# Kernel tuning notes

Hardware: AMD Instinct MI355X
Metric: run time of the kernel (lower is better)

## Reference

```python
import jax, jax.numpy as jnp
import numpy as np

D_IN, D_HID, D_OUT = 256, 256, 10  # mlp dims (init_kwargs)


def mlp(params, x):
    # x: [D_IN] (single sample, matching fnet_single's unsqueeze/squeeze)
    h = jnp.tanh(x @ params["W1"] + params["b1"])
    h = jnp.tanh(h @ params["W2"] + params["b2"])
    return h @ params["W3"] + params["b3"]  # [D_OUT]


def setup_inputs() -> dict:
    key = jax.random.key(0)
    ks = jax.random.split(key, 8)
    rn = lambda k, shp, scale: (jax.random.normal(k, shp, jnp.float32) * scale)
    return {
        "x1": jax.random.normal(ks[0], (64, D_IN), jnp.float32),
        "x2": jax.random.normal(ks[1], (64, D_IN), jnp.float32),
        "W1": rn(ks[2], (D_IN, D_HID), 1.0 / np.sqrt(D_IN)),
        "b1": jnp.zeros((D_HID,), jnp.float32),
        "W2": rn(ks[3], (D_HID, D_HID), 1.0 / np.sqrt(D_HID)),
        "b2": jnp.zeros((D_HID,), jnp.float32),
        "W3": rn(ks[4], (D_HID, D_OUT), 1.0 / np.sqrt(D_HID)),
        "b3": jnp.zeros((D_OUT,), jnp.float32),
    }


def reference(x1, x2, W1, b1, W2, b2, W3, b3):
    params = {"W1": W1, "b1": b1, "W2": W2, "b2": b2, "W3": W3, "b3": b3}
    # vmap(jacrev(fnet_single), (None, 0)): per-sample Jacobian w.r.t. every param tensor
    jac_fn = jax.vmap(jax.jacrev(mlp, argnums=0), in_axes=(None, 0))
    jac1 = jax.tree_util.tree_leaves(jac_fn(params, x1))  # list of [N, O, *pshape]
    jac2 = jax.tree_util.tree_leaves(jac_fn(params, x2))  # list of [M, O, *pshape]
    # flatten(2): [N, O, f] per param tensor
    j1 = [j.reshape(j.shape[0], j.shape[1], -1) for j in jac1]
    j2 = [j.reshape(j.shape[0], j.shape[1], -1) for j in jac2]
    # per-param einsum, then sum over param tensors (== stack(...).sum(0))
    result = sum(jnp.einsum("Naf,Mbf->NMab", a, b) for a, b in zip(j1, j2))
    return result  # [N, M, O, O]
```

## Files before the change

### kernel.cpp

```cpp
#include <hip/hip_runtime.h>

#define NS 64
#define D  256
#define O  10

typedef unsigned short u16;
typedef __attribute__((ext_vector_type(8))) short bf16x8;
typedef __attribute__((ext_vector_type(4))) float f32x4;

__device__ __forceinline__ u16 f2bf(float f) {
    union { float f; unsigned u; } v; v.f = f;
    unsigned r = v.u + 0x7FFFu + ((v.u >> 16) & 1u);
    return (u16)(r >> 16);
}
__device__ __forceinline__ float bf2f(u16 h) {
    union { unsigned u; float f; } v; v.u = ((unsigned)h) << 16;
    return v.f;
}

__global__ __launch_bounds__(512) void prep1_kernel(
    const float* __restrict__ x1, const float* __restrict__ x2,
    const float* __restrict__ W1, const float* __restrict__ b1,
    const float* __restrict__ W2, const float* __restrict__ b2,
    const float* __restrict__ W3,
    float* __restrict__ h1o, float* __restrict__ S1o,
    float* __restrict__ h2o, u16* __restrict__ G2b,
    float* __restrict__ W2T)
{
    int t = threadIdx.x;
    if (blockIdx.x >= 128) {
        int blk = blockIdx.x - 128;
        int bxT = blk & 7, byT = blk >> 3;
        __shared__ float tile[32][33];
        int txT = t & 31, tyT = t >> 5;
        #pragma unroll
        for (int r = 0; r < 2; ++r)
            tile[tyT + 16 * r][txT] = W2[(byT * 32 + tyT + 16 * r) * D + bxT * 32 + txT];
        __syncthreads();
        #pragma unroll
        for (int r = 0; r < 2; ++r)
            W2T[(bxT * 32 + tyT + 16 * r) * D + byT * 32 + txT] = tile[txT][tyT + 16 * r];
        return;
    }

    int s = blockIdx.x;
    const float* x = (s < NS) ? (x1 + s * D) : (x2 + (s - NS) * D);
    int tt = t & 255, half = t >> 8;
    int k0 = half * 128;
    __shared__ float xs[D];
    __shared__ float hs[D];
    __shared__ float part[2][D];

    if (half == 0) xs[tt] = x[tt];
    __syncthreads();

    float acc = half ? 0.0f : b1[tt];
    #pragma unroll 8
    for (int k = 0; k < 128; ++k) acc = fmaf(xs[k0 + k], W1[(k0 + k) * D + tt], acc);
    part[half][tt] = acc;
    __syncthreads();

    if (half == 0) {
        float h1v = tanhf(part[0][tt] + part[1][tt]);
        h1o[s * D + tt] = h1v;
        S1o[s * D + tt] = 1.0f - h1v * h1v;
        hs[tt] = h1v;
    }
    __syncthreads();

    acc = half ? 0.0f : b2[tt];
    #pragma unroll 8
    for (int k = 0; k < 128; ++k) acc = fmaf(hs[k0 + k], W2[(k0 + k) * D + tt], acc);
    part[half][tt] = acc;
    __syncthreads();

    if (half == 0) {
        float h2v = tanhf(part[0][tt] + part[1][tt]);
        h2o[s * D + tt] = h2v;
        hs[tt] = 1.0f - h2v * h2v;
    }
    __syncthreads();

    for (int idx = t; idx < O * D; idx += 512) {
        int a = idx >> 8, i = idx & 255;
        G2b[(s * O + a) * D + i] = f2bf(hs[i] * W3[i * O + a]);
    }
}

__global__ __launch_bounds__(512) void prep2_kernel(
    const float* __restrict__ W2T, const float* __restrict__ S1,
    const u16* __restrict__ G2b, u16* __restrict__ G1b,
    const float* __restrict__ x1, const float* __restrict__ x2,
    const float* __restrict__ h1, const float* __restrict__ h2,
    float* __restrict__ dots)
{
    int t = threadIdx.x;
    if (blockIdx.x < 128) {
        int s = blockIdx.x;
        __shared__ float g2s[O * D];
        __shared__ float red[O * D];
        for (int idx = t; idx < D * O; idx += 512) g2s[idx] = bf2f(G2b[s * D * O + idx]);
        __syncthreads();

        int tt = t & 255, half = t >> 8;
        int j0 = half * 128;
        float acc[O];
        #pragma unroll
        for (int a = 0; a < O; ++a) acc[a] = 0.0f;
        #pragma unroll 2
        for (int j = 0; j < 128; j += 4) {
            float w0 = W2T[(j0 + j + 0) * D + tt];
            float w1 = W2T[(j0 + j + 1) * D + tt];
            float w2 = W2T[(j0 + j + 2) * D + tt];
            float w3 = W2T[(j0 + j + 3) * D + tt];
            #pragma unroll
            for (int a = 0; a < O; ++a) {
                float4 g = *(const float4*)&g2s[a * D + j0 + j];
                acc[a] = fmaf(w0, g.x, acc[a]);
                acc[a] = fmaf(w1, g.y, acc[a]);
                acc[a] = fmaf(w2, g.z, acc[a]);
                acc[a] = fmaf(w3, g.w, acc[a]);
            }
        }
        if (half == 1) {
            #pragma unroll
            for (int a = 0; a < O; ++a) red[a * D + tt] = acc[a];
        }
        __syncthreads();
        if (half == 0) {
            float s1 = S1[s * D + tt];
            #pragma unroll
            for (int a = 0; a < O; ++a)
                G1b[(s * O + a) * D + tt] = f2bf(s1 * (acc[a] + red[a * D + tt]));
        }
        return;
    }

    int idx = blockIdx.x - 128;
    int which = idx >> 6, n = idx & 63;
    const float* A; const float* B;
    if (which == 0)      { A = x1 + n * D; B = x2; }
    else if (which == 1) { A = h1 + n * D; B = h1 + NS * D; }
    else                 { A = h2 + n * D; B = h2 + NS * D; }
    __shared__ float as[D];
    if (t < D) as[t] = A[t];
    __syncthreads();
    int wave = t >> 6, lane = t & 63;
    for (int m = wave; m < NS; m += 8) {
        const float* Bv = B + m * D;
        float v = as[lane] * Bv[lane]
                + as[64 + lane] * Bv[64 + lane]
                + as[128 + lane] * Bv[128 + lane]
                + as[192 + lane] * Bv[192 + lane];
        #pragma unroll
        for (int off = 32; off > 0; off >>= 1) v += __shfl_xor(v, off);
        if (lane == 0) dots[(which * NS + n) * NS + m] = v;
    }
}

__global__ __launch_bounds__(64) void ntk_mfma_kernel(
    const u16* __restrict__ G1b, const u16* __restrict__ G2b,
    const float* __restrict__ dots, float* __restrict__ out)
{
    int lane = threadIdx.x;
    int by = blockIdx.x / 40, bx = blockIdx.x % 40;
    int R0 = by * 16, C0 = bx * 16;
    int lm = lane & 15;
    int lk = (lane >> 4) * 8;

    const u16* a1p = G1b + (R0 + lm) * D + lk;
    const u16* b1p = G1b + (640 + C0 + lm) * D + lk;
    const u16* a2p = G2b + (R0 + lm) * D + lk;
    const u16* b2p = G2b + (640 + C0 + lm) * D + lk;

    f32x4 acc1 = {0.f, 0.f, 0.f, 0.f}, acc2 = {0.f, 0.f, 0.f, 0.f};
    #pragma unroll
    for (int ks = 0; ks < 8; ++ks) {
        bf16x8 a1 = *(const bf16x8*)(a1p + ks * 32);
        bf16x8 b1 = *(const bf16x8*)(b1p + ks * 32);
        bf16x8 a2 = *(const bf16x8*)(a2p + ks * 32);
        bf16x8 b2 = *(const bf16x8*)(b2p + ks * 32);
        acc1 = __builtin_amdgcn_mfma_f32_16x16x32_bf16(a1, b1, acc1, 0, 0, 0);
        acc2 = __builtin_amdgcn_mfma_f32_16x16x32_bf16(a2, b2, acc2, 0, 0, 0);
    }

    int C = C0 + lm;
    int m = C / 10, b = C - m * 10;
    #pragma unroll
    for (int r = 0; r < 4; ++r) {
        int R = R0 + (lane >> 4) * 4 + r;
        int n = R / 10, a = R - n * 10;
        float cx  = 1.0f + dots[0 * NS * NS + n * NS + m];
        float ch1 = 1.0f + dots[1 * NS * NS + n * NS + m];
        float val = cx * acc1[r] + ch1 * acc2[r];
        if (a == b) val += 1.0f + dots[2 * NS * NS + n * NS + m];
        out[(n * NS + m) * (O * O) + a * O + b] = val;
    }
}

extern "C" void kernel_launch(void* const* d_in, const int* in_sizes, int n_in,
                              void* d_out, int out_size, void* d_ws, size_t ws_size,
                              hipStream_t stream) {
    const float* x1 = (const float*)d_in[0];
    const float* x2 = (const float*)d_in[1];
    const float* W1 = (const float*)d_in[2];
    const float* b1 = (const float*)d_in[3];
    const float* W2 = (const float*)d_in[4];
    const float* b2 = (const float*)d_in[5];
    const float* W3 = (const float*)d_in[6];

    float* ws   = (float*)d_ws;
    float* h1   = ws;
    float* S1   = h1 + 128 * D;
    float* h2   = S1 + 128 * D;
    float* W2T  = h2 + 128 * D;
    float* dots = W2T + D * D;
    u16*  G2b   = (u16*)(dots + 3 * NS * NS);
    u16*  G1b   = G2b + 1280 * D;
    float* out  = (float*)d_out;

    hipLaunchKernelGGL(prep1_kernel, dim3(192), dim3(512), 0, stream,
                       x1, x2, W1, b1, W2, b2, W3, h1, S1, h2, G2b, W2T);
    hipLaunchKernelGGL(prep2_kernel, dim3(320), dim3(512), 0, stream,
                       W2T, S1, G2b, G1b, x1, x2, h1, h2, dots);
    hipLaunchKernelGGL(ntk_mfma_kernel, dim3(1600), dim3(64), 0, stream,
                       G1b, G2b, dots, out);
}
```

Before: 101.5 us.

## Split prep stages into three kernels with per-half-output blocks for more parallelism

Replaces the two prep kernels with separate layer-1 forward, layer-2 forward and backward kernels. Each uses 256-thread blocks that each compute half of a sample's outputs, which doubles the number of blocks per sample. The three dot-product sets are spread across these kernels so each one runs alongside the stage that produces its inputs. The goal is higher occupancy and shorter per-block serial chains on a small problem. The cost is one extra kernel launch and an extra global round trip for h1.

```diff
diff --git a/kernel.cpp b/kernel.cpp
--- a/kernel.cpp
+++ b/kernel.cpp
@@ -18,135 +18,15 @@
     return v.f;
 }
 
-__global__ __launch_bounds__(512) void prep1_kernel(
-    const float* __restrict__ x1, const float* __restrict__ x2,
-    const float* __restrict__ W1, const float* __restrict__ b1,
-    const float* __restrict__ W2, const float* __restrict__ b2,
-    const float* __restrict__ W3,
-    float* __restrict__ h1o, float* __restrict__ S1o,
-    float* __restrict__ h2o, u16* __restrict__ G2b,
-    float* __restrict__ W2T)
-{
-    int t = threadIdx.x;
-    if (blockIdx.x >= 128) {
-        int blk = blockIdx.x - 128;
-        int bxT = blk & 7, byT = blk >> 3;
-        __shared__ float tile[32][33];
-        int txT = t & 31, tyT = t >> 5;
-        #pragma unroll
-        for (int r = 0; r < 2; ++r)
-            tile[tyT + 16 * r][txT] = W2[(byT * 32 + tyT + 16 * r) * D + bxT * 32 + txT];
-        __syncthreads();
-        #pragma unroll
-        for (int r = 0; r < 2; ++r)
-            W2T[(bxT * 32 + tyT + 16 * r) * D + byT * 32 + txT] = tile[txT][tyT + 16 * r];
-        return;
-    }
-
-    int s = blockIdx.x;
-    const float* x = (s < NS) ? (x1 + s * D) : (x2 + (s - NS) * D);
-    int tt = t & 255, half = t >> 8;
-    int k0 = half * 128;
-    __shared__ float xs[D];
-    __shared__ float hs[D];
-    __shared__ float part[2][D];
-
-    if (half == 0) xs[tt] = x[tt];
-    __syncthreads();
-
-    float acc = half ? 0.0f : b1[tt];
-    #pragma unroll 8
-    for (int k = 0; k < 128; ++k) acc = fmaf(xs[k0 + k], W1[(k0 + k) * D + tt], acc);
-    part[half][tt] = acc;
-    __syncthreads();
-
-    if (half == 0) {
-        float h1v = tanhf(part[0][tt] + part[1][tt]);
-        h1o[s * D + tt] = h1v;
-        S1o[s * D + tt] = 1.0f - h1v * h1v;
-        hs[tt] = h1v;
-    }
-    __syncthreads();
-
-    acc = half ? 0.0f : b2[tt];
-    #pragma unroll 8
-    for (int k = 0; k < 128; ++k) acc = fmaf(hs[k0 + k], W2[(k0 + k) * D + tt], acc);
-    part[half][tt] = acc;
-    __syncthreads();
-
-    if (half == 0) {
-        float h2v = tanhf(part[0][tt] + part[1][tt]);
-        h2o[s * D + tt] = h2v;
-        hs[tt] = 1.0f - h2v * h2v;
-    }
-    __syncthreads();
-
-    for (int idx = t; idx < O * D; idx += 512) {
-        int a = idx >> 8, i = idx & 255;
-        G2b[(s * O + a) * D + i] = f2bf(hs[i] * W3[i * O + a]);
-    }
-}
-
-__global__ __launch_bounds__(512) void prep2_kernel(
-    const float* __restrict__ W2T, const float* __restrict__ S1,
-    const u16* __restrict__ G2b, u16* __restrict__ G1b,
-    const float* __restrict__ x1, const float* __restrict__ x2,
-    const float* __restrict__ h1, const float* __restrict__ h2,
-    float* __restrict__ dots)
-{
-    int t = threadIdx.x;
-    if (blockIdx.x < 128) {
-        int s = blockIdx.x;
-        __shared__ float g2s[O * D];
-        __shared__ float red[O * D];
-        for (int idx = t; idx < D * O; idx += 512) g2s[idx] = bf2f(G2b[s * D * O + idx]);
-        __syncthreads();
-
-        int tt = t & 255, half = t >> 8;
-        int j0 = half * 128;
-        float acc[O];
-        #pragma unroll
-        for (int a = 0; a < O; ++a) acc[a] = 0.0f;
-        #pragma unroll 2
-        for (int j = 0; j < 128; j += 4) {
-            float w0 = W2T[(j0 + j + 0) * D + tt];
-            float w1 = W2T[(j0 + j + 1) * D + tt];
-            float w2 = W2T[(j0 + j + 2) * D + tt];
-            float w3 = W2T[(j0 + j + 3) * D + tt];
-            #pragma unroll
-            for (int a = 0; a < O; ++a) {
-                float4 g = *(const float4*)&g2s[a * D + j0 + j];
-                acc[a] = fmaf(w0, g.x, acc[a]);
-                acc[a] = fmaf(w1, g.y, acc[a]);
-                acc[a] = fmaf(w2, g.z, acc[a]);
-                acc[a] = fmaf(w3, g.w, acc[a]);
-            }
-        }
-        if (half == 1) {
-            #pragma unroll
-            for (int a = 0; a < O; ++a) red[a * D + tt] = acc[a];
-        }
-        __syncthreads();
-        if (half == 0) {
-            float s1 = S1[s * D + tt];
-            #pragma unroll
-            for (int a = 0; a < O; ++a)
-                G1b[(s * O + a) * D + tt] = f2bf(s1 * (acc[a] + red[a * D + tt]));
-        }
-        return;
-    }
-
-    int idx = blockIdx.x - 128;
-    int which = idx >> 6, n = idx & 63;
-    const float* A; const float* B;
-    if (which == 0)      { A = x1 + n * D; B = x2; }
-    else if (which == 1) { A = h1 + n * D; B = h1 + NS * D; }
-    else                 { A = h2 + n * D; B = h2 + NS * D; }
+__device__ __forceinline__ void dots_block(const float* __restrict__ A,
+                                           const float* __restrict__ B,
+                                           float* __restrict__ dst, int t)
+{
     __shared__ float as[D];
-    if (t < D) as[t] = A[t];
+    as[t] = A[t];
     __syncthreads();
     int wave = t >> 6, lane = t & 63;
-    for (int m = wave; m < NS; m += 8) {
+    for (int m = wave; m < NS; m += 4) {
         const float* Bv = B + m * D;
         float v = as[lane] * Bv[lane]
                 + as[64 + lane] * Bv[64 + lane]
@@ -154,7 +34,143 @@
                 + as[192 + lane] * Bv[192 + lane];
         #pragma unroll
         for (int off = 32; off > 0; off >>= 1) v += __shfl_xor(v, off);
-        if (lane == 0) dots[(which * NS + n) * NS + m] = v;
+        if (lane == 0) dst[m] = v;
+    }
+}
+
+__global__ __launch_bounds__(256) void fwd1_kernel(
+    const float* __restrict__ x1, const float* __restrict__ x2,
+    const float* __restrict__ W1, const float* __restrict__ b1,
+    const float* __restrict__ W2,
+    float* __restrict__ h1o, float* __restrict__ S1o,
+    float* __restrict__ W2T, float* __restrict__ dots)
+{
+    int t = threadIdx.x, b = blockIdx.x;
+    if (b >= 320) {
+        int n = b - 320;
+        dots_block(x1 + n * D, x2, dots + 0 * NS * NS + n * NS, t);
+        return;
+    }
+    if (b >= 256) {
+        int blk = b - 256;
+        int bxT = blk & 7, byT = blk >> 3;
+        __shared__ float tile[32][33];
+        int txT = t & 31, tyT = t >> 5;
+        #pragma unroll
+        for (int r = 0; r < 4; ++r)
+            tile[tyT + 8 * r][txT] = W2[(byT * 32 + tyT + 8 * r) * D + bxT * 32 + txT];
+        __syncthreads();
+        #pragma unroll
+        for (int r = 0; r < 4; ++r)
+            W2T[(bxT * 32 + tyT + 8 * r) * D + byT * 32 + txT] = tile[txT][tyT + 8 * r];
+        return;
+    }
+
+    int s = b >> 1, oh = b & 1;
+    const float* x = (s < NS) ? (x1 + s * D) : (x2 + (s - NS) * D);
+    int jj = t & 127, kh = t >> 7;
+    int j = oh * 128 + jj, k0 = kh * 128;
+    __shared__ float xs[D];
+    __shared__ float part[128];
+    xs[t] = x[t];
+    __syncthreads();
+
+    float acc = kh ? 0.0f : b1[j];
+    #pragma unroll 8
+    for (int k = 0; k < 128; ++k) acc = fmaf(xs[k0 + k], W1[(k0 + k) * D + j], acc);
+    if (kh) part[jj] = acc;
+    __syncthreads();
+    if (!kh) {
+        float h1v = tanhf(acc + part[jj]);
+        h1o[s * D + j] = h1v;
+        S1o[s * D + j] = 1.0f - h1v * h1v;
+    }
+}
+
+__global__ __launch_bounds__(256) void fwd2_kernel(
+    const float* __restrict__ h1, const float* __restrict__ W2,
+    const float* __restrict__ b2, const float* __restrict__ W3,
+    float* __restrict__ h2o, u16* __restrict__ G2b,
+    float* __restrict__ dots)
+{
+    int t = threadIdx.x, b = blockIdx.x;
+    if (b >= 256) {
+        int n = b - 256;
+        dots_block(h1 + n * D, h1 + NS * D, dots + 1 * NS * NS + n * NS, t);
+        return;
+    }
+
+    int s = b >> 1, oh = b & 1;
+    int jj = t & 127, kh = t >> 7;
+    int j = oh * 128 + jj, k0 = kh * 128;
+    __shared__ float hs[D];
+    __shared__ float part[128];
+    hs[t] = h1[s * D + t];
+    __syncthreads();
+
+    float acc = kh ? 0.0f : b2[j];
+    #pragma unroll 8
+    for (int k = 0; k < 128; ++k) acc = fmaf(hs[k0 + k], W2[(k0 + k) * D + j], acc);
+    if (kh) part[jj] = acc;
+    __syncthreads();
+    if (!kh) {
+        float h2v = tanhf(acc + part[jj]);
+        h2o[s * D + j] = h2v;
+        float s2 = 1.0f - h2v * h2v;
+        #pragma unroll
+        for (int a = 0; a < O; ++a)
+            G2b[(s * O + a) * D + j] = f2bf(s2 * W3[j * O + a]);
+    }
+}
+
+__global__ __launch_bounds__(256) void bwd_kernel(
+    const float* __restrict__ W2T, const float* __restrict__ S1,
+    const u16* __restrict__ G2b, u16* __restrict__ G1b,
+    const float* __restrict__ h2, float* __restrict__ dots)
+{
+    int t = threadIdx.x, b = blockIdx.x;
+    if (b >= 256) {
+        int n = b - 256;
+        dots_block(h2 + n * D, h2 + NS * D, dots + 2 * NS * NS + n * NS, t);
+        return;
+    }
+
+    int s = b >> 1, ih = b & 1;
+    int ii = t & 127, jh = t >> 7;
+    int i = ih * 128 + ii, j0 = jh * 128;
+    __shared__ float g2s[O * D];
+    __shared__ float red[O * 128];
+    for (int idx = t; idx < O * D; idx += 256) g2s[idx] = bf2f(G2b[s * O * D + idx]);
+    __syncthreads();
+
+    float acc[O];
+    #pragma unroll
+    for (int a = 0; a < O; ++a) acc[a] = 0.0f;
+    #pragma unroll 2
+    for (int j = 0; j < 128; j += 4) {
+        float w0 = W2T[(j0 + j + 0) * D + i];
+        float w1 = W2T[(j0 + j + 1) * D + i];
+        float w2 = W2T[(j0 + j + 2) * D + i];
+        float w3 = W2T[(j0 + j + 3) * D + i];
+        #pragma unroll
+        for (int a = 0; a < O; ++a) {
+            float4 g = *(const float4*)&g2s[a * D + j0 + j];
+            acc[a] = fmaf(w0, g.x, acc[a]);
+            acc[a] = fmaf(w1, g.y, acc[a]);
+            acc[a] = fmaf(w2, g.z, acc[a]);
+            acc[a] = fmaf(w3, g.w, acc[a]);
+        }
+    }
+    if (jh) {
+        #pragma unroll
+        for (int a = 0; a < O; ++a) red[a * 128 + ii] = acc[a];
+    }
+    __syncthreads();
+    if (!jh) {
+        float s1v = S1[s * D + i];
+        #pragma unroll
+        for (int a = 0; a < O; ++a)
+            G1b[(s * O + a) * D + i] = f2bf(s1v * (acc[a] + red[a * 128 + ii]));
     }
 }
 
@@ -219,10 +235,12 @@
     u16*  G1b   = G2b + 1280 * D;
     float* out  = (float*)d_out;
 
-    hipLaunchKernelGGL(prep1_kernel, dim3(192), dim3(512), 0, stream,
-                       x1, x2, W1, b1, W2, b2, W3, h1, S1, h2, G2b, W2T);
-    hipLaunchKernelGGL(prep2_kernel, dim3(320), dim3(512), 0, stream,
-                       W2T, S1, G2b, G1b, x1, x2, h1, h2, dots);
+    hipLaunchKernelGGL(fwd1_kernel, dim3(384), dim3(256), 0, stream,
+                       x1, x2, W1, b1, W2, h1, S1, W2T, dots);
+    hipLaunchKernelGGL(fwd2_kernel, dim3(320), dim3(256), 0, stream,
+                       h1, W2, b2, W3, h2, G2b, dots);
+    hipLaunchKernelGGL(bwd_kernel, dim3(320), dim3(256), 0, stream,
+                       W2T, S1, G2b, G1b, h2, dots);
     hipLaunchKernelGGL(ntk_mfma_kernel, dim3(1600), dim3(64), 0, stream,
                        G1b, G2b, dots, out);
 }
```

New measurement: 107.1 us. 1.06x slower.
